# Kernel optimization log

Measured on AMD Instinct MI355X. Metric: run time of the kernel, lower is better.

The kernel has to match this reference:

```python
import jax, jax.numpy as jnp
import numpy as np

N_NODES = 100000

def _sage(x, src, tgt, Wl, bl, Wr):
    # PyG SAGEConv (mean aggr): out = lin_l(mean_{j in N(i)} x_j) + lin_r(x_i)
    msg = x[src]                                             # [E, F] gather
    s = jax.ops.segment_sum(msg, tgt, num_segments=N_NODES)  # [N, F]
    cnt = jax.ops.segment_sum(jnp.ones((src.shape[0], 1), x.dtype), tgt, num_segments=N_NODES)
    agg = s / jnp.maximum(cnt, 1.0)
    return agg @ Wl + bl + x @ Wr


def setup_inputs() -> dict:
    key = jax.random.key(0)
    ks = jax.random.split(key, 16)
    node_dim, edge_dim, hidden = 128, 16, 64
    E = 1000000
    x = jax.random.normal(ks[0], (N_NODES, node_dim), jnp.float32)
    edge_index = jax.random.randint(ks[1], (2, E), 0, N_NODES, jnp.int64)
    edge_attr = jax.random.normal(ks[2], (E, edge_dim), jnp.float32)
    def lin(k, fi, fo, scale=None):
        s = scale if scale is not None else 1.0 / np.sqrt(fi)
        return jax.random.uniform(k, (fi, fo), jnp.float32, -s, s)
    return {
        "x": x, "edge_index": edge_index, "edge_attr": edge_attr,
        # edge MLP: Linear(16,64) -> ReLU -> Linear(64,64)
        "We1": lin(ks[3], edge_dim, hidden), "be1": jnp.zeros((hidden,), jnp.float32),
        "We2": lin(ks[4], hidden, hidden),   "be2": jnp.zeros((hidden,), jnp.float32),
        # SAGEConv 0: lin_l (with bias, on aggregated) + lin_r (no bias, on root)
        "Wl0": lin(ks[5], node_dim, hidden), "bl0": jnp.zeros((hidden,), jnp.float32),
        "Wr0": lin(ks[6], node_dim, hidden),
        # SAGEConv 1
        "Wl1": lin(ks[7], hidden, hidden), "bl1": jnp.zeros((hidden,), jnp.float32),
        "Wr1": lin(ks[8], hidden, hidden),
        # output MLP: Linear(64,64) -> ReLU -> (Dropout eval=id) -> Linear(64,1)
        "Wo1": lin(ks[9], hidden, hidden), "bo1": jnp.zeros((hidden,), jnp.float32),
        "Wo2": lin(ks[10], hidden, 1),     "bo2": jnp.zeros((1,), jnp.float32),
    }


def reference(x, edge_index, edge_attr, We1, be1, We2, be2,
              Wl0, bl0, Wr0, Wl1, bl1, Wr1, Wo1, bo1, Wo2, bo2):
    src, tgt = edge_index[0], edge_index[1]
    # edge MLP (dropout in eval mode = identity)
    ea = jax.nn.relu(edge_attr @ We1 + be1) @ We2 + be2       # [E, H]
    # two SAGE layers with ReLU
    h = jax.nn.relu(_sage(x, src, tgt, Wl0, bl0, Wr0))        # [N, H]
    h = jax.nn.relu(_sage(h, src, tgt, Wl1, bl1, Wr1))        # [N, H]
    # per-edge features: gather both endpoints + edge embedding
    ef = h[src] + h[tgt] + ea                                 # [E, H]
    out = jax.nn.relu(ef @ Wo1 + bo1) @ Wo2 + bo2             # [E, 1]
    return jax.nn.sigmoid(out[:, 0])                          # [E]
```

## Files before the change

kernel.cpp:

```cpp
#include <hip/hip_runtime.h>
#include <math.h>

typedef __attribute__((ext_vector_type(8))) short short8;
typedef __attribute__((ext_vector_type(4))) float f32x4;

#define CAPB 4096

static __device__ __forceinline__ unsigned short f2bf(float f) {
  union { float f; unsigned int u; } x; x.f = f;
  unsigned int r = x.u + 0x7fffu + ((x.u >> 16) & 1u);
  return (unsigned short)(r >> 16);
}
static __device__ __forceinline__ float bf2f(unsigned int u) {
  union { unsigned int u; float f; } x; x.u = u << 16; return x.f;
}

__global__ __launch_bounds__(256) void k_pre(
    const unsigned int* __restrict__ w, int nSample,
    unsigned int* __restrict__ flag, int* __restrict__ gcursor,
    const float* __restrict__ Wl0, const float* __restrict__ Wr0,
    const float* __restrict__ Wl1, const float* __restrict__ Wr1,
    unsigned short* __restrict__ WnT1, unsigned short* __restrict__ WnT0) {
  const int tid = threadIdx.x;
  const int b = blockIdx.x;
  if (b == 0) {
    gcursor[tid] = 0; gcursor[tid + 256] = 0;
    __shared__ unsigned int red[256];
    unsigned int v = 0;
    for (int i = tid; i < nSample; i += 256) v |= w[2 * i + 1];
    red[tid] = v;
    __syncthreads();
    for (int s = 128; s > 0; s >>= 1) {
      if (tid < s) red[tid] |= red[tid + s];
      __syncthreads();
    }
    if (tid == 0) flag[0] = red[0];
  } else if (b <= 32) {
    int idx = (b - 1) * 256 + tid;
    int n = idx >> 6, k = idx & 63;
    float v = (n < 64) ? Wl1[(size_t)k * 64 + n] : Wr1[(size_t)k * 64 + (n - 64)];
    WnT1[idx] = f2bf(v);
  } else {
    int idx = (b - 33) * 256 + tid;
    int n = idx >> 7, k = idx & 127;
    float v = (n < 64) ? Wl0[(size_t)k * 64 + n] : Wr0[(size_t)k * 64 + (n - 64)];
    WnT0[idx] = f2bf(v);
  }
}

template <int K, bool BF16IN, int NTILES>
__device__ __forceinline__ void ngemm_body(
    const void* __restrict__ Xv, const unsigned short* __restrict__ WnT,
    unsigned short* __restrict__ Y0, unsigned short* __restrict__ Y1,
    int N, int blk, unsigned short* __restrict__ sX) {
  constexpr int STR = K + 8;
  constexpr int NC = K / 32;
  const int tid = threadIdx.x;
  const int wv = tid >> 6, lane = tid & 63;
  const int m = lane & 15, q = lane >> 4;
  const int row0 = blk * 64;

  short8 bB[NTILES][NC];
#pragma unroll
  for (int ct = 0; ct < NTILES; ++ct)
#pragma unroll
    for (int c = 0; c < NC; ++c) {
      int n = (NTILES == 2) ? (wv * 32 + ct * 16 + m) : (wv * 16 + m);
      bB[ct][c] = *(const short8*)(WnT + (size_t)n * K + c * 32 + q * 8);
    }

#pragma unroll
  for (int i = 0; i < K / 16; ++i) {
    int f = tid + 256 * i;
    int r = f / (K / 4);
    int c4 = f % (K / 4);
    int rr = row0 + r; if (rr >= N) rr = N - 1;
    uint2 pk;
    if constexpr (BF16IN) {
      pk = *(const uint2*)((const unsigned short*)Xv + (size_t)rr * K + c4 * 4);
    } else {
      float4 v = *(const float4*)((const float*)Xv + (size_t)rr * K + c4 * 4);
      pk.x = (unsigned int)f2bf(v.x) | ((unsigned int)f2bf(v.y) << 16);
      pk.y = (unsigned int)f2bf(v.z) | ((unsigned int)f2bf(v.w) << 16);
    }
    *(uint2*)(sX + r * STR + c4 * 4) = pk;
  }
  __syncthreads();

  f32x4 acc[4][NTILES];
#pragma unroll
  for (int rt = 0; rt < 4; ++rt)
#pragma unroll
    for (int ct = 0; ct < NTILES; ++ct)
#pragma unroll
      for (int r = 0; r < 4; ++r) acc[rt][ct][r] = 0.f;

#pragma unroll
  for (int c = 0; c < NC; ++c) {
    short8 a[4];
#pragma unroll
    for (int rt = 0; rt < 4; ++rt)
      a[rt] = *(const short8*)(sX + (rt * 16 + m) * STR + c * 32 + q * 8);
#pragma unroll
    for (int rt = 0; rt < 4; ++rt)
#pragma unroll
      for (int ct = 0; ct < NTILES; ++ct)
        acc[rt][ct] = __builtin_amdgcn_mfma_f32_16x16x32_bf16(a[rt], bB[ct][c], acc[rt][ct], 0, 0, 0);
  }

#pragma unroll
  for (int rt = 0; rt < 4; ++rt)
#pragma unroll
    for (int ct = 0; ct < NTILES; ++ct) {
      unsigned short* Yw;
      int n;
      if constexpr (NTILES == 2) {
        Yw = (wv < 2) ? Y0 : Y1;
        n = (wv & 1) * 32 + ct * 16 + m;
      } else {
        Yw = Y0;
        n = wv * 16 + m;
      }
#pragma unroll
      for (int reg = 0; reg < 4; ++reg) {
        int row = row0 + rt * 16 + q * 4 + reg;
        if (row < N) Yw[(size_t)row * 64 + n] = f2bf(acc[rt][ct][reg]);
      }
    }
}

template <int K, bool BF16IN, int NTILES>
__global__ __launch_bounds__(256) void k_ngemm(
    const void* __restrict__ Xv, const unsigned short* __restrict__ WnT,
    unsigned short* __restrict__ Y0, unsigned short* __restrict__ Y1, int N) {
  __shared__ __align__(16) unsigned short sX[64 * (K + 8)];
  ngemm_body<K, BF16IN, NTILES>(Xv, WnT, Y0, Y1, N, blockIdx.x, sX);
}

__global__ __launch_bounds__(256) void k_mega1(
    const unsigned int* __restrict__ w, const unsigned int* __restrict__ flag,
    int E, int nDec, int gB,
    int* __restrict__ src, int* __restrict__ tgt,
    int* __restrict__ gcursor, unsigned int* __restrict__ tmp,
    const float* __restrict__ x, const unsigned short* __restrict__ WnT0,
    unsigned short* __restrict__ Yl, unsigned short* __restrict__ Yr, int N,
    const float* __restrict__ We2, const float* __restrict__ Wo1,
    const float* __restrict__ be2, const float* __restrict__ bo1,
    const float* __restrict__ We1,
    unsigned short* __restrict__ W25T, unsigned short* __restrict__ We1T,
    unsigned short* __restrict__ Wo1T, float* __restrict__ cvec,
    const float4* __restrict__ ef, uint2* __restrict__ eb) {
  __shared__ __align__(16) char smem[64 * 136 * 2];
  const int tid = threadIdx.x;
  const int wi = blockIdx.x;

  if (wi < gB) {
    ngemm_body<128, false, 2>(x, WnT0, Yl, Yr, N, wi, (unsigned short*)smem);
    return;
  }
  if (wi < gB + nDec) {
    const int di = wi - gB;
    int* hist = (int*)smem;
    hist[tid] = 0; hist[tid + 256] = 0;
    __syncthreads();
    const int e0 = di * 2048;
    const int e1 = (e0 + 2048 < E) ? (e0 + 2048) : E;
    const unsigned int fl = flag[0];
    for (int e = e0 + tid; e < e1; e += 256) {
      int s, t;
      if (fl) { s = (int)w[e]; t = (int)w[E + e]; }
      else    { s = (int)w[2 * e]; t = (int)w[2 * (E + e)]; }
      src[e] = s; tgt[e] = t;
      atomicAdd(hist + (t >> 8), 1);
    }
    __syncthreads();
    {
      int c0 = hist[tid], c1 = hist[tid + 256];
      int s0 = (c0 > 0) ? atomicAdd(gcursor + tid, c0) : 0;
      int s1 = (c1 > 0) ? atomicAdd(gcursor + tid + 256, c1) : 0;
      __syncthreads();
      hist[tid] = s0; hist[tid + 256] = s1;
    }
    __syncthreads();
    for (int e = e0 + tid; e < e1; e += 256) {
      int s, t;
      if (fl) { s = (int)w[e]; t = (int)w[E + e]; }
      else    { s = (int)w[2 * e]; t = (int)w[2 * (E + e)]; }
      int b = t >> 8;
      int pos = atomicAdd(hist + b, 1);
      if (pos < CAPB)
        tmp[(size_t)b * CAPB + pos] = ((unsigned int)s << 8) | (unsigned int)(t & 255);
    }
    return;
  }
  if (wi == gB + nDec) {
    float* sB = (float*)smem;
    for (int i = tid; i < 1024; i += 256)
      *(float4*)&sB[i * 4] = *(const float4*)(Wo1 + i * 4);
    __syncthreads();
    for (int idx = tid; idx < 4096; idx += 256) {
      int k = idx >> 6, n = idx & 63;
      float s = 0.f;
#pragma unroll 8
      for (int mm = 0; mm < 64; ++mm) s = fmaf(We2[k * 64 + mm], sB[mm * 64 + n], s);
      W25T[n * 64 + k] = f2bf(s);
      Wo1T[n * 64 + k] = f2bf(sB[k * 64 + n]);
    }
    for (int idx = tid; idx < 2048; idx += 256) {
      int n = idx >> 5, k = idx & 31;
      We1T[n * 32 + k] = (k < 16) ? f2bf(We1[k * 64 + n]) : (unsigned short)0;
    }
    if (tid < 64) {
      float s = bo1[tid];
#pragma unroll 8
      for (int mm = 0; mm < 64; ++mm) s = fmaf(be2[mm], sB[mm * 64 + tid], s);
      cvec[tid] = s;
    }
    return;
  }
  const int ci = wi - (gB + nDec + 1);
  const int nItems = E * 4;
#pragma unroll
  for (int j = 0; j < 4; ++j) {
    int i = ci * 1024 + j * 256 + tid;
    if (i < nItems) {
      float4 v = ef[i];
      uint2 pk;
      pk.x = (unsigned int)f2bf(v.x) | ((unsigned int)f2bf(v.y) << 16);
      pk.y = (unsigned int)f2bf(v.z) | ((unsigned int)f2bf(v.w) << 16);
      eb[i] = pk;
    }
  }
}

__global__ __launch_bounds__(256) void k_bsort(
    const unsigned int* __restrict__ tmp, const int* __restrict__ gcursor,
    int* __restrict__ csrc, uint2* __restrict__ rowptr2, int N) {
  __shared__ int cnt[256];
  __shared__ int curs[256];
  __shared__ int wsum[4];
  const int b = blockIdx.x, tid = threadIdx.x;
  int c = gcursor[b]; if (c > CAPB) c = CAPB;
  cnt[tid] = 0;
  __syncthreads();
  const unsigned int* reg = tmp + (size_t)b * CAPB;
  for (int i = tid; i < c; i += 256) atomicAdd(&cnt[reg[i] & 255u], 1);
  __syncthreads();
  const int lane = tid & 63, wv = tid >> 6;
  int v = cnt[tid];
  int incl = v;
#pragma unroll
  for (int off = 1; off < 64; off <<= 1) {
    int t = __shfl_up(incl, off, 64);
    if (lane >= off) incl += t;
  }
  if (lane == 63) wsum[wv] = incl;
  __syncthreads();
  int add = 0;
  for (int ww = 0; ww < wv; ++ww) add += wsum[ww];
  int excl = add + incl - v;
  curs[tid] = excl;
  int node = b * 256 + tid;
  if (node < N)
    rowptr2[node] = make_uint2((unsigned int)(b * CAPB + excl),
                               (unsigned int)(b * CAPB + excl + v));
  __syncthreads();
  for (int i = tid; i < c; i += 256) {
    unsigned int wd = reg[i];
    int p = atomicAdd(&curs[wd & 255u], 1);
    csrc[(size_t)b * CAPB + p] = (int)(wd >> 8);
  }
}

__global__ __launch_bounds__(256) void k_agg(
    const unsigned short* __restrict__ Y, const uint2* __restrict__ rowptr2,
    const int* __restrict__ csrc, const float* __restrict__ bias,
    const unsigned short* __restrict__ Yr, unsigned short* __restrict__ H,
    int N) {
  int node = (blockIdx.x * 256 + threadIdx.x) >> 6;
  if (node >= N) return;
  const int lane = threadIdx.x & 63;
  const int c4 = lane & 15, rr = lane >> 4;
  uint2 be = rowptr2[node];
  int beg = (int)be.x, end = (int)be.y;
  float a0 = 0.f, a1 = 0.f, a2 = 0.f, a3 = 0.f;
  float b0 = 0.f, b1 = 0.f, b2 = 0.f, b3 = 0.f;
  for (int e = beg; e < end; e += 8) {
    int e0 = e + rr, e1 = e + 4 + rr;
    if (e0 < end) {
      int s = csrc[e0];
      uint2 v = *(const uint2*)(Y + (size_t)s * 64 + c4 * 4);
      a0 += bf2f(v.x & 0xffffu); a1 += bf2f(v.x >> 16);
      a2 += bf2f(v.y & 0xffffu); a3 += bf2f(v.y >> 16);
    }
    if (e1 < end) {
      int s = csrc[e1];
      uint2 v = *(const uint2*)(Y + (size_t)s * 64 + c4 * 4);
      b0 += bf2f(v.x & 0xffffu); b1 += bf2f(v.x >> 16);
      b2 += bf2f(v.y & 0xffffu); b3 += bf2f(v.y >> 16);
    }
  }
  a0 += b0; a1 += b1; a2 += b2; a3 += b3;
#pragma unroll
  for (int msk = 16; msk <= 32; msk <<= 1) {
    a0 += __shfl_xor(a0, msk, 64);
    a1 += __shfl_xor(a1, msk, 64);
    a2 += __shfl_xor(a2, msk, 64);
    a3 += __shfl_xor(a3, msk, 64);
  }
  if (rr == 0) {
    float cdeg = (float)(end - beg);
    if (cdeg < 1.f) cdeg = 1.f;
    float inv = 1.f / cdeg;
    float4 bv = *(const float4*)(bias + c4 * 4);
    uint2 yv = *(const uint2*)(Yr + (size_t)node * 64 + c4 * 4);
    float o0 = fmaxf(a0 * inv + bv.x + bf2f(yv.x & 0xffffu), 0.f);
    float o1 = fmaxf(a1 * inv + bv.y + bf2f(yv.x >> 16), 0.f);
    float o2 = fmaxf(a2 * inv + bv.z + bf2f(yv.y & 0xffffu), 0.f);
    float o3 = fmaxf(a3 * inv + bv.w + bf2f(yv.y >> 16), 0.f);
    uint2 pk;
    pk.x = (unsigned int)f2bf(o0) | ((unsigned int)f2bf(o1) << 16);
    pk.y = (unsigned int)f2bf(o2) | ((unsigned int)f2bf(o3) << 16);
    *(uint2*)(H + (size_t)node * 64 + c4 * 4) = pk;
  }
}

#define T1_STRIDE 72
#define G_STRIDE 68
__global__ __launch_bounds__(256) void k_edge3(
    const unsigned short* __restrict__ EAb, const int* __restrict__ src,
    const int* __restrict__ tgt, const unsigned short* __restrict__ Gb,
    const unsigned short* __restrict__ We1T,
    const unsigned short* __restrict__ W25T,
    const float* __restrict__ cvec, const float* __restrict__ be1,
    const float* __restrict__ Wo2, const float* __restrict__ bo2,
    float* __restrict__ out, int E, int nT, int nWaves) {
  __shared__ __align__(16) char sBuf[4][4352];
  const int tid = threadIdx.x;
  const int wid = tid >> 6, lane = tid & 63;
  const int m = lane & 15, q = lane >> 4;
  unsigned short* sT1 = (unsigned short*)sBuf[wid];
  float* sG = (float*)sBuf[wid];

  short8 bWe1[4], bW25[4][2];
  float cv[4], wo2v[4], be1v[4];
#pragma unroll
  for (int nt = 0; nt < 4; ++nt) {
    int n = nt * 16 + m;
    bWe1[nt] = *(const short8*)(We1T + n * 32 + q * 8);
    bW25[nt][0] = *(const short8*)(W25T + n * 64 + q * 8);
    bW25[nt][1] = *(const short8*)(W25T + n * 64 + 32 + q * 8);
    cv[nt] = cvec[n];
    wo2v[nt] = Wo2[n];
    be1v[nt] = be1[n];
  }
  const float b_out = bo2[0];
  const short8 zfrag = {};

  int t = blockIdx.x * 4 + wid;
  if (t >= nT) return;

  uint2 sv[4], tv[4];
  {
    int il = t * 16 + m; if (il >= E) il = E - 1;
    int my = (lane < 16) ? src[il] : ((lane < 32) ? tgt[il] : 0);
#pragma unroll
    for (int r = 0; r < 4; ++r) {
      int a = __shfl(my, q * 4 + r, 64);
      int b = __shfl(my, 16 + q * 4 + r, 64);
      sv[r] = *(const uint2*)(Gb + (size_t)a * 64 + m * 4);
      tv[r] = *(const uint2*)(Gb + (size_t)b * 64 + m * 4);
    }
  }

  while (true) {
    const int base = t * 16;
    const int tn = t + nWaves;
    const bool last = (tn >= nT);
    const int tc = last ? t : tn;

    int il_n = tc * 16 + m; if (il_n >= E) il_n = E - 1;
    int idx_n = (lane < 16) ? src[il_n] : ((lane < 32) ? tgt[il_n] : 0);
    uint2 sv_n[4], tv_n[4];
#pragma unroll
    for (int r = 0; r < 4; ++r) {
      int a = __shfl(idx_n, q * 4 + r, 64);
      int b = __shfl(idx_n, 16 + q * 4 + r, 64);
      sv_n[r] = *(const uint2*)(Gb + (size_t)a * 64 + m * 4);
      tv_n[r] = *(const uint2*)(Gb + (size_t)b * 64 + m * 4);
    }

    int er = base + m; if (er >= E) er = E - 1;
    short8 aEA = zfrag;
    if (q < 2) aEA = *(const short8*)(EAb + (size_t)er * 16 + (q & 1) * 8);

    f32x4 t1[4];
#pragma unroll
    for (int nt = 0; nt < 4; ++nt) {
      f32x4 cinit; cinit[0] = be1v[nt]; cinit[1] = be1v[nt];
      cinit[2] = be1v[nt]; cinit[3] = be1v[nt];
      t1[nt] = __builtin_amdgcn_mfma_f32_16x16x32_bf16(aEA, bWe1[nt], cinit, 0, 0, 0);
    }
#pragma unroll
    for (int nt = 0; nt < 4; ++nt)
#pragma unroll
      for (int r = 0; r < 4; ++r)
        sT1[(q * 4 + r) * T1_STRIDE + nt * 16 + m] = f2bf(fmaxf(t1[nt][r], 0.f));
    short8 aT0 = *(short8*)(sT1 + m * T1_STRIDE + q * 8);
    short8 aT1 = *(short8*)(sT1 + m * T1_STRIDE + 32 + q * 8);

#pragma unroll
    for (int r = 0; r < 4; ++r) {
      f32x4 g;
      g[0] = bf2f(sv[r].x & 0xffffu) + bf2f(tv[r].x & 0xffffu);
      g[1] = bf2f(sv[r].x >> 16)     + bf2f(tv[r].x >> 16);
      g[2] = bf2f(sv[r].y & 0xffffu) + bf2f(tv[r].y & 0xffffu);
      g[3] = bf2f(sv[r].y >> 16)     + bf2f(tv[r].y >> 16);
      *(f32x4*)(sG + (q * 4 + r) * G_STRIDE + m * 4) = g;
    }

    f32x4 acc[4];
#pragma unroll
    for (int nt = 0; nt < 4; ++nt)
#pragma unroll
      for (int r = 0; r < 4; ++r)
        acc[nt][r] = cv[nt] + sG[(q * 4 + r) * G_STRIDE + nt * 16 + m];
#pragma unroll
    for (int nt = 0; nt < 4; ++nt) {
      acc[nt] = __builtin_amdgcn_mfma_f32_16x16x32_bf16(aT0, bW25[nt][0], acc[nt], 0, 0, 0);
      acc[nt] = __builtin_amdgcn_mfma_f32_16x16x32_bf16(aT1, bW25[nt][1], acc[nt], 0, 0, 0);
    }

    float p[4];
#pragma unroll
    for (int r = 0; r < 4; ++r) {
      p[r] = fmaxf(acc[0][r], 0.f) * wo2v[0] + fmaxf(acc[1][r], 0.f) * wo2v[1] +
             fmaxf(acc[2][r], 0.f) * wo2v[2] + fmaxf(acc[3][r], 0.f) * wo2v[3];
    }
#pragma unroll
    for (int msk = 1; msk <= 8; msk <<= 1) {
#pragma unroll
      for (int r = 0; r < 4; ++r) p[r] += __shfl_xor(p[r], msk, 64);
    }
    if (m == 0) {
#pragma unroll
      for (int r = 0; r < 4; ++r) {
        int row = base + q * 4 + r;
        if (row < E) out[row] = 1.f / (1.f + __expf(-(p[r] + b_out)));
      }
    }

    if (last) break;
    t = tn;
#pragma unroll
    for (int r = 0; r < 4; ++r) { sv[r] = sv_n[r]; tv[r] = tv_n[r]; }
  }
}

extern "C" void kernel_launch(void* const* d_in, const int* in_sizes, int n_in,
                              void* d_out, int out_size, void* d_ws, size_t ws_size,
                              hipStream_t stream) {
  const float* x     = (const float*)d_in[0];
  const unsigned int* eidx = (const unsigned int*)d_in[1];
  const float* eattr = (const float*)d_in[2];
  const float* We1 = (const float*)d_in[3];
  const float* be1 = (const float*)d_in[4];
  const float* We2 = (const float*)d_in[5];
  const float* be2 = (const float*)d_in[6];
  const float* Wl0 = (const float*)d_in[7];
  const float* bl0 = (const float*)d_in[8];
  const float* Wr0 = (const float*)d_in[9];
  const float* Wl1 = (const float*)d_in[10];
  const float* bl1 = (const float*)d_in[11];
  const float* Wr1 = (const float*)d_in[12];
  const float* Wo1 = (const float*)d_in[13];
  const float* bo1 = (const float*)d_in[14];
  const float* Wo2 = (const float*)d_in[15];
  const float* bo2 = (const float*)d_in[16];

  const int N = in_sizes[0] / 128;
  const int E = in_sizes[2] / 16;
  const int NBUCK = (N + 255) >> 8;
  float* out = (float*)d_out;

  char* ws = (char*)d_ws;
  size_t off = 0;
  auto alloc = [&](size_t bytes) {
    char* p = ws + off;
    off += (bytes + 255) & ~(size_t)255;
    return p;
  };
  unsigned int* flag = (unsigned int*)alloc(256);
  int* src    = (int*)alloc((size_t)E * 4);
  int* tgt    = (int*)alloc((size_t)E * 4);
  int* gcursor = (int*)alloc(512 * 4);
  unsigned int* tmp = (unsigned int*)alloc((size_t)NBUCK * CAPB * 4);
  int* csrc   = (int*)alloc((size_t)NBUCK * CAPB * 4);
  uint2* rowptr2 = (uint2*)alloc((size_t)N * 8);
  unsigned short* EAb = (unsigned short*)alloc((size_t)E * 16 * 2);
  unsigned short* Hb = (unsigned short*)alloc((size_t)N * 64 * 2);
  unsigned short* Yl = (unsigned short*)alloc((size_t)N * 64 * 2);
  unsigned short* Yr = (unsigned short*)alloc((size_t)N * 64 * 2);
  unsigned short* Gb = (unsigned short*)alloc((size_t)N * 64 * 2);
  unsigned short* W25T = (unsigned short*)alloc(64 * 64 * 2);
  unsigned short* We1T = (unsigned short*)alloc(64 * 32 * 2);
  unsigned short* Wo1T = (unsigned short*)alloc(64 * 64 * 2);
  unsigned short* WnT1 = (unsigned short*)alloc(128 * 64 * 2);
  unsigned short* WnT0 = (unsigned short*)alloc(128 * 128 * 2);
  float* cvec = (float*)alloc(64 * 4);
  (void)ws_size; (void)n_in; (void)out_size;

  const int nDec = (E + 2047) / 2048;
  const int gB = (N + 63) / 64;
  const int nConv = (E * 4 + 1023) / 1024;

  k_pre<<<97, 256, 0, stream>>>(eidx, 8192, flag, gcursor,
                                Wl0, Wr0, Wl1, Wr1, WnT1, WnT0);

  k_mega1<<<gB + nDec + 1 + nConv, 256, 0, stream>>>(
      eidx, flag, E, nDec, gB,
      src, tgt, gcursor, tmp,
      x, WnT0, Yl, Yr, N,
      We2, Wo1, be2, bo1, We1,
      W25T, We1T, Wo1T, cvec,
      (const float4*)eattr, (uint2*)EAb);

  k_bsort<<<NBUCK, 256, 0, stream>>>(tmp, gcursor, csrc, rowptr2, N);

  const int aggB = (N + 3) / 4;
  k_agg<<<aggB, 256, 0, stream>>>(Yl, rowptr2, csrc, bl0, Yr, Hb, N);

  k_ngemm<64, true, 2><<<gB, 256, 0, stream>>>(Hb, WnT1, Yl, Yr, N);
  k_agg<<<aggB, 256, 0, stream>>>(Yl, rowptr2, csrc, bl1, Yr, Hb, N);

  k_ngemm<64, true, 1><<<gB, 256, 0, stream>>>(Hb, Wo1T, Gb, nullptr, N);

  const int nT = (E + 15) / 16;
  const int blocks = 3072;
  k_edge3<<<blocks, 256, 0, stream>>>(EAb, src, tgt, Gb, We1T, W25T, cvec,
                                      be1, Wo2, bo2, out, E, nT, blocks * 4);
}
```

Baseline: 429.6 us.

## Fuse SAGE mean aggregation with following node GEMM and drop edge gather prefetch

Mean-neighbour aggregation is merged with the next dense bf16 MFMA projection in one kernel. Aggregated rows go into shared memory instead of an H buffer in global memory, which removes two launches and an N×64 write and read per layer, with new ping-pong Yl2/Yr2 buffers. Each wave now aggregates 16 nodes one after another, so there is less parallelism across nodes and 64-row blocks may be load-imbalanced. The edge kernel stops prefetching next-tile Gb rows into registers and loads them in the same iteration, lowering register pressure but exposing gather latency; it also splits its shared buffer into separate T1 and G arrays.

```diff
diff --git a/kernel.cpp b/kernel.cpp
--- a/kernel.cpp
+++ b/kernel.cpp
@@ -129,14 +129,6 @@
     }
 }
 
-template <int K, bool BF16IN, int NTILES>
-__global__ __launch_bounds__(256) void k_ngemm(
-    const void* __restrict__ Xv, const unsigned short* __restrict__ WnT,
-    unsigned short* __restrict__ Y0, unsigned short* __restrict__ Y1, int N) {
-  __shared__ __align__(16) unsigned short sX[64 * (K + 8)];
-  ngemm_body<K, BF16IN, NTILES>(Xv, WnT, Y0, Y1, N, blockIdx.x, sX);
-}
-
 __global__ __launch_bounds__(256) void k_mega1(
     const unsigned int* __restrict__ w, const unsigned int* __restrict__ flag,
     int E, int nDec, int gB,
@@ -272,57 +264,122 @@
   }
 }
 
-__global__ __launch_bounds__(256) void k_agg(
+template <int NTILES>
+__global__ __launch_bounds__(256) void k_fagg(
     const unsigned short* __restrict__ Y, const uint2* __restrict__ rowptr2,
     const int* __restrict__ csrc, const float* __restrict__ bias,
-    const unsigned short* __restrict__ Yr, unsigned short* __restrict__ H,
-    int N) {
-  int node = (blockIdx.x * 256 + threadIdx.x) >> 6;
-  if (node >= N) return;
-  const int lane = threadIdx.x & 63;
-  const int c4 = lane & 15, rr = lane >> 4;
-  uint2 be = rowptr2[node];
-  int beg = (int)be.x, end = (int)be.y;
-  float a0 = 0.f, a1 = 0.f, a2 = 0.f, a3 = 0.f;
-  float b0 = 0.f, b1 = 0.f, b2 = 0.f, b3 = 0.f;
-  for (int e = beg; e < end; e += 8) {
-    int e0 = e + rr, e1 = e + 4 + rr;
-    if (e0 < end) {
-      int s = csrc[e0];
-      uint2 v = *(const uint2*)(Y + (size_t)s * 64 + c4 * 4);
-      a0 += bf2f(v.x & 0xffffu); a1 += bf2f(v.x >> 16);
-      a2 += bf2f(v.y & 0xffffu); a3 += bf2f(v.y >> 16);
-    }
-    if (e1 < end) {
-      int s = csrc[e1];
-      uint2 v = *(const uint2*)(Y + (size_t)s * 64 + c4 * 4);
-      b0 += bf2f(v.x & 0xffffu); b1 += bf2f(v.x >> 16);
-      b2 += bf2f(v.y & 0xffffu); b3 += bf2f(v.y >> 16);
-    }
-  }
-  a0 += b0; a1 += b1; a2 += b2; a3 += b3;
-#pragma unroll
-  for (int msk = 16; msk <= 32; msk <<= 1) {
-    a0 += __shfl_xor(a0, msk, 64);
-    a1 += __shfl_xor(a1, msk, 64);
-    a2 += __shfl_xor(a2, msk, 64);
-    a3 += __shfl_xor(a3, msk, 64);
-  }
-  if (rr == 0) {
-    float cdeg = (float)(end - beg);
-    if (cdeg < 1.f) cdeg = 1.f;
-    float inv = 1.f / cdeg;
-    float4 bv = *(const float4*)(bias + c4 * 4);
-    uint2 yv = *(const uint2*)(Yr + (size_t)node * 64 + c4 * 4);
-    float o0 = fmaxf(a0 * inv + bv.x + bf2f(yv.x & 0xffffu), 0.f);
-    float o1 = fmaxf(a1 * inv + bv.y + bf2f(yv.x >> 16), 0.f);
-    float o2 = fmaxf(a2 * inv + bv.z + bf2f(yv.y & 0xffffu), 0.f);
-    float o3 = fmaxf(a3 * inv + bv.w + bf2f(yv.y >> 16), 0.f);
-    uint2 pk;
-    pk.x = (unsigned int)f2bf(o0) | ((unsigned int)f2bf(o1) << 16);
-    pk.y = (unsigned int)f2bf(o2) | ((unsigned int)f2bf(o3) << 16);
-    *(uint2*)(H + (size_t)node * 64 + c4 * 4) = pk;
-  }
+    const unsigned short* __restrict__ Yr, const unsigned short* __restrict__ WnT,
+    unsigned short* __restrict__ Y0, unsigned short* __restrict__ Y1, int N) {
+  constexpr int K = 64;
+  constexpr int STR = K + 8;
+  constexpr int NC = K / 32;
+  __shared__ __align__(16) unsigned short sX[64 * STR];
+  const int tid = threadIdx.x;
+  const int wv = tid >> 6, lane = tid & 63;
+  const int m = lane & 15, q = lane >> 4;
+  const int row0 = blockIdx.x * 64;
+
+  short8 bB[NTILES][NC];
+#pragma unroll
+  for (int ct = 0; ct < NTILES; ++ct)
+#pragma unroll
+    for (int c = 0; c < NC; ++c) {
+      int n = (NTILES == 2) ? (wv * 32 + ct * 16 + m) : (wv * 16 + m);
+      bB[ct][c] = *(const short8*)(WnT + (size_t)n * K + c * 32 + q * 8);
+    }
+
+  {
+    int nb = row0 + wv * 16 + m; if (nb >= N) nb = N - 1;
+    uint2 myrp = rowptr2[nb];
+    float4 bv = *(const float4*)(bias + m * 4);
+    for (int i = 0; i < 16; ++i) {
+      int r = wv * 16 + i;
+      int node = row0 + r; if (node >= N) node = N - 1;
+      int beg = __shfl((int)myrp.x, i, 16);
+      int end = __shfl((int)myrp.y, i, 16);
+      float a0 = 0.f, a1 = 0.f, a2 = 0.f, a3 = 0.f;
+      float b0 = 0.f, b1 = 0.f, b2 = 0.f, b3 = 0.f;
+      for (int e = beg; e < end; e += 8) {
+        int e0 = e + q, e1 = e + 4 + q;
+        if (e0 < end) {
+          int s = csrc[e0];
+          uint2 v = *(const uint2*)(Y + (size_t)s * 64 + m * 4);
+          a0 += bf2f(v.x & 0xffffu); a1 += bf2f(v.x >> 16);
+          a2 += bf2f(v.y & 0xffffu); a3 += bf2f(v.y >> 16);
+        }
+        if (e1 < end) {
+          int s = csrc[e1];
+          uint2 v = *(const uint2*)(Y + (size_t)s * 64 + m * 4);
+          b0 += bf2f(v.x & 0xffffu); b1 += bf2f(v.x >> 16);
+          b2 += bf2f(v.y & 0xffffu); b3 += bf2f(v.y >> 16);
+        }
+      }
+      a0 += b0; a1 += b1; a2 += b2; a3 += b3;
+#pragma unroll
+      for (int msk = 16; msk <= 32; msk <<= 1) {
+        a0 += __shfl_xor(a0, msk, 64);
+        a1 += __shfl_xor(a1, msk, 64);
+        a2 += __shfl_xor(a2, msk, 64);
+        a3 += __shfl_xor(a3, msk, 64);
+      }
+      if (q == 0) {
+        float cdeg = (float)(end - beg);
+        if (cdeg < 1.f) cdeg = 1.f;
+        float inv = 1.f / cdeg;
+        uint2 yv = *(const uint2*)(Yr + (size_t)node * 64 + m * 4);
+        float o0 = fmaxf(a0 * inv + bv.x + bf2f(yv.x & 0xffffu), 0.f);
+        float o1 = fmaxf(a1 * inv + bv.y + bf2f(yv.x >> 16), 0.f);
+        float o2 = fmaxf(a2 * inv + bv.z + bf2f(yv.y & 0xffffu), 0.f);
+        float o3 = fmaxf(a3 * inv + bv.w + bf2f(yv.y >> 16), 0.f);
+        uint2 pk;
+        pk.x = (unsigned int)f2bf(o0) | ((unsigned int)f2bf(o1) << 16);
+        pk.y = (unsigned int)f2bf(o2) | ((unsigned int)f2bf(o3) << 16);
+        *(uint2*)(sX + r * STR + m * 4) = pk;
+      }
+    }
+  }
+  __syncthreads();
+
+  f32x4 acc[4][NTILES];
+#pragma unroll
+  for (int rt = 0; rt < 4; ++rt)
+#pragma unroll
+    for (int ct = 0; ct < NTILES; ++ct)
+#pragma unroll
+      for (int r = 0; r < 4; ++r) acc[rt][ct][r] = 0.f;
+
+#pragma unroll
+  for (int c = 0; c < NC; ++c) {
+    short8 a[4];
+#pragma unroll
+    for (int rt = 0; rt < 4; ++rt)
+      a[rt] = *(const short8*)(sX + (rt * 16 + m) * STR + c * 32 + q * 8);
+#pragma unroll
+    for (int rt = 0; rt < 4; ++rt)
+#pragma unroll
+      for (int ct = 0; ct < NTILES; ++ct)
+        acc[rt][ct] = __builtin_amdgcn_mfma_f32_16x16x32_bf16(a[rt], bB[ct][c], acc[rt][ct], 0, 0, 0);
+  }
+
+#pragma unroll
+  for (int rt = 0; rt < 4; ++rt)
+#pragma unroll
+    for (int ct = 0; ct < NTILES; ++ct) {
+      unsigned short* Yw;
+      int n;
+      if constexpr (NTILES == 2) {
+        Yw = (wv < 2) ? Y0 : Y1;
+        n = (wv & 1) * 32 + ct * 16 + m;
+      } else {
+        Yw = Y0;
+        n = wv * 16 + m;
+      }
+#pragma unroll
+      for (int reg = 0; reg < 4; ++reg) {
+        int row = row0 + rt * 16 + q * 4 + reg;
+        if (row < N) Yw[(size_t)row * 64 + n] = f2bf(acc[rt][ct][reg]);
+      }
+    }
 }
 
 #define T1_STRIDE 72
@@ -335,12 +392,13 @@
     const float* __restrict__ cvec, const float* __restrict__ be1,
     const float* __restrict__ Wo2, const float* __restrict__ bo2,
     float* __restrict__ out, int E, int nT, int nWaves) {
-  __shared__ __align__(16) char sBuf[4][4352];
+  __shared__ unsigned short sT1a[4][16 * T1_STRIDE];
+  __shared__ float sGa[4][16 * G_STRIDE];
   const int tid = threadIdx.x;
   const int wid = tid >> 6, lane = tid & 63;
   const int m = lane & 15, q = lane >> 4;
-  unsigned short* sT1 = (unsigned short*)sBuf[wid];
-  float* sG = (float*)sBuf[wid];
+  unsigned short* sT1 = sT1a[wid];
+  float* sG = sGa[wid];
 
   short8 bWe1[4], bW25[4][2];
   float cv[4], wo2v[4], be1v[4];
@@ -359,19 +417,8 @@
 
   int t = blockIdx.x * 4 + wid;
   if (t >= nT) return;
-
-  uint2 sv[4], tv[4];
-  {
-    int il = t * 16 + m; if (il >= E) il = E - 1;
-    int my = (lane < 16) ? src[il] : ((lane < 32) ? tgt[il] : 0);
-#pragma unroll
-    for (int r = 0; r < 4; ++r) {
-      int a = __shfl(my, q * 4 + r, 64);
-      int b = __shfl(my, 16 + q * 4 + r, 64);
-      sv[r] = *(const uint2*)(Gb + (size_t)a * 64 + m * 4);
-      tv[r] = *(const uint2*)(Gb + (size_t)b * 64 + m * 4);
-    }
-  }
+  int il = t * 16 + m; if (il >= E) il = E - 1;
+  int my_idx = (lane < 16) ? src[il] : ((lane < 32) ? tgt[il] : 0);
 
   while (true) {
     const int base = t * 16;
@@ -381,13 +428,18 @@
 
     int il_n = tc * 16 + m; if (il_n >= E) il_n = E - 1;
     int idx_n = (lane < 16) ? src[il_n] : ((lane < 32) ? tgt[il_n] : 0);
-    uint2 sv_n[4], tv_n[4];
+
+    int rs[4], rt[4];
 #pragma unroll
     for (int r = 0; r < 4; ++r) {
-      int a = __shfl(idx_n, q * 4 + r, 64);
-      int b = __shfl(idx_n, 16 + q * 4 + r, 64);
-      sv_n[r] = *(const uint2*)(Gb + (size_t)a * 64 + m * 4);
-      tv_n[r] = *(const uint2*)(Gb + (size_t)b * 64 + m * 4);
+      rs[r] = __shfl(my_idx, q * 4 + r, 64);
+      rt[r] = __shfl(my_idx, 16 + q * 4 + r, 64);
+    }
+    uint2 sv[4], tv[4];
+#pragma unroll
+    for (int r = 0; r < 4; ++r) {
+      sv[r] = *(const uint2*)(Gb + (size_t)rs[r] * 64 + m * 4);
+      tv[r] = *(const uint2*)(Gb + (size_t)rt[r] * 64 + m * 4);
     }
 
     int er = base + m; if (er >= E) er = E - 1;
@@ -451,9 +503,7 @@
     }
 
     if (last) break;
-    t = tn;
-#pragma unroll
-    for (int r = 0; r < 4; ++r) { sv[r] = sv_n[r]; tv[r] = tv_n[r]; }
+    t = tn; my_idx = idx_n;
   }
 }
 
@@ -498,9 +548,10 @@
   int* csrc   = (int*)alloc((size_t)NBUCK * CAPB * 4);
   uint2* rowptr2 = (uint2*)alloc((size_t)N * 8);
   unsigned short* EAb = (unsigned short*)alloc((size_t)E * 16 * 2);
-  unsigned short* Hb = (unsigned short*)alloc((size_t)N * 64 * 2);
   unsigned short* Yl = (unsigned short*)alloc((size_t)N * 64 * 2);
   unsigned short* Yr = (unsigned short*)alloc((size_t)N * 64 * 2);
+  unsigned short* Yl2 = (unsigned short*)alloc((size_t)N * 64 * 2);
+  unsigned short* Yr2 = (unsigned short*)alloc((size_t)N * 64 * 2);
   unsigned short* Gb = (unsigned short*)alloc((size_t)N * 64 * 2);
   unsigned short* W25T = (unsigned short*)alloc(64 * 64 * 2);
   unsigned short* We1T = (unsigned short*)alloc(64 * 32 * 2);
@@ -527,13 +578,10 @@
 
   k_bsort<<<NBUCK, 256, 0, stream>>>(tmp, gcursor, csrc, rowptr2, N);
 
-  const int aggB = (N + 3) / 4;
-  k_agg<<<aggB, 256, 0, stream>>>(Yl, rowptr2, csrc, bl0, Yr, Hb, N);
-
-  k_ngemm<64, true, 2><<<gB, 256, 0, stream>>>(Hb, WnT1, Yl, Yr, N);
-  k_agg<<<aggB, 256, 0, stream>>>(Yl, rowptr2, csrc, bl1, Yr, Hb, N);
-
-  k_ngemm<64, true, 1><<<gB, 256, 0, stream>>>(Hb, Wo1T, Gb, nullptr, N);
+  k_fagg<2><<<gB, 256, 0, stream>>>(Yl, rowptr2, csrc, bl0, Yr, WnT1,
+                                    Yl2, Yr2, N);
+  k_fagg<1><<<gB, 256, 0, stream>>>(Yl2, rowptr2, csrc, bl1, Yr2, Wo1T,
+                                    Gb, nullptr, N);
 
   const int nT = (E + 15) / 16;
   const int blocks = 3072;
```

Result: no change. 431.7 us (+0.5%).

## Fuse bucket sort into aggregation using LDS float atomics per bucket half

Applied to the files above, without the earlier changes.

Drops the CSR build kernel (k_bsort) and the per-node gather aggregation. A new k_bagg kernel scans each 256-node bucket's edge list directly and accumulates neighbour features into shared memory with float atomics, split across two blocks per bucket (128 nodes each). It then writes mean+bias+root output. This removes a kernel launch and the csrc/rowptr writes and reads, at the cost of each half-block reading the whole bucket list and heavy LDS atomic contention. Floating-point summation order also becomes nondeterministic. Separately, the edge kernel drops its register-level prefetch of the next tile's gathered rows and uses split LDS buffers.

```diff
diff --git a/kernel.cpp b/kernel.cpp
--- a/kernel.cpp
+++ b/kernel.cpp
@@ -233,95 +233,72 @@
   }
 }
 
-__global__ __launch_bounds__(256) void k_bsort(
+__global__ __launch_bounds__(256) void k_bagg(
     const unsigned int* __restrict__ tmp, const int* __restrict__ gcursor,
-    int* __restrict__ csrc, uint2* __restrict__ rowptr2, int N) {
-  __shared__ int cnt[256];
-  __shared__ int curs[256];
-  __shared__ int wsum[4];
-  const int b = blockIdx.x, tid = threadIdx.x;
-  int c = gcursor[b]; if (c > CAPB) c = CAPB;
-  cnt[tid] = 0;
-  __syncthreads();
-  const unsigned int* reg = tmp + (size_t)b * CAPB;
-  for (int i = tid; i < c; i += 256) atomicAdd(&cnt[reg[i] & 255u], 1);
-  __syncthreads();
-  const int lane = tid & 63, wv = tid >> 6;
-  int v = cnt[tid];
-  int incl = v;
-#pragma unroll
-  for (int off = 1; off < 64; off <<= 1) {
-    int t = __shfl_up(incl, off, 64);
-    if (lane >= off) incl += t;
-  }
-  if (lane == 63) wsum[wv] = incl;
-  __syncthreads();
-  int add = 0;
-  for (int ww = 0; ww < wv; ++ww) add += wsum[ww];
-  int excl = add + incl - v;
-  curs[tid] = excl;
-  int node = b * 256 + tid;
-  if (node < N)
-    rowptr2[node] = make_uint2((unsigned int)(b * CAPB + excl),
-                               (unsigned int)(b * CAPB + excl + v));
-  __syncthreads();
-  for (int i = tid; i < c; i += 256) {
-    unsigned int wd = reg[i];
-    int p = atomicAdd(&curs[wd & 255u], 1);
-    csrc[(size_t)b * CAPB + p] = (int)(wd >> 8);
-  }
-}
-
-__global__ __launch_bounds__(256) void k_agg(
-    const unsigned short* __restrict__ Y, const uint2* __restrict__ rowptr2,
-    const int* __restrict__ csrc, const float* __restrict__ bias,
+    const unsigned short* __restrict__ Y, const float* __restrict__ bias,
     const unsigned short* __restrict__ Yr, unsigned short* __restrict__ H,
     int N) {
-  int node = (blockIdx.x * 256 + threadIdx.x) >> 6;
-  if (node >= N) return;
-  const int lane = threadIdx.x & 63;
-  const int c4 = lane & 15, rr = lane >> 4;
-  uint2 be = rowptr2[node];
-  int beg = (int)be.x, end = (int)be.y;
-  float a0 = 0.f, a1 = 0.f, a2 = 0.f, a3 = 0.f;
-  float b0 = 0.f, b1 = 0.f, b2 = 0.f, b3 = 0.f;
-  for (int e = beg; e < end; e += 8) {
-    int e0 = e + rr, e1 = e + 4 + rr;
-    if (e0 < end) {
-      int s = csrc[e0];
-      uint2 v = *(const uint2*)(Y + (size_t)s * 64 + c4 * 4);
-      a0 += bf2f(v.x & 0xffffu); a1 += bf2f(v.x >> 16);
-      a2 += bf2f(v.y & 0xffffu); a3 += bf2f(v.y >> 16);
-    }
-    if (e1 < end) {
-      int s = csrc[e1];
-      uint2 v = *(const uint2*)(Y + (size_t)s * 64 + c4 * 4);
-      b0 += bf2f(v.x & 0xffffu); b1 += bf2f(v.x >> 16);
-      b2 += bf2f(v.y & 0xffffu); b3 += bf2f(v.y >> 16);
-    }
-  }
-  a0 += b0; a1 += b1; a2 += b2; a3 += b3;
-#pragma unroll
-  for (int msk = 16; msk <= 32; msk <<= 1) {
-    a0 += __shfl_xor(a0, msk, 64);
-    a1 += __shfl_xor(a1, msk, 64);
-    a2 += __shfl_xor(a2, msk, 64);
-    a3 += __shfl_xor(a3, msk, 64);
-  }
-  if (rr == 0) {
-    float cdeg = (float)(end - beg);
-    if (cdeg < 1.f) cdeg = 1.f;
-    float inv = 1.f / cdeg;
-    float4 bv = *(const float4*)(bias + c4 * 4);
-    uint2 yv = *(const uint2*)(Yr + (size_t)node * 64 + c4 * 4);
-    float o0 = fmaxf(a0 * inv + bv.x + bf2f(yv.x & 0xffffu), 0.f);
-    float o1 = fmaxf(a1 * inv + bv.y + bf2f(yv.x >> 16), 0.f);
-    float o2 = fmaxf(a2 * inv + bv.z + bf2f(yv.y & 0xffffu), 0.f);
-    float o3 = fmaxf(a3 * inv + bv.w + bf2f(yv.y >> 16), 0.f);
-    uint2 pk;
-    pk.x = (unsigned int)f2bf(o0) | ((unsigned int)f2bf(o1) << 16);
-    pk.y = (unsigned int)f2bf(o2) | ((unsigned int)f2bf(o3) << 16);
-    *(uint2*)(H + (size_t)node * 64 + c4 * 4) = pk;
+  __shared__ float acc[128 * 65];
+  __shared__ int cnt[128];
+  const int tid = threadIdx.x;
+  const int b = blockIdx.x >> 1, h = blockIdx.x & 1;
+  const int g = tid >> 4, m = tid & 15;
+  for (int i = tid; i < 128 * 65; i += 256) acc[i] = 0.f;
+  if (tid < 128) cnt[tid] = 0;
+  __syncthreads();
+
+  int c = gcursor[b]; if (c > CAPB) c = CAPB;
+  const unsigned int* reg = tmp + (size_t)b * CAPB;
+  for (int e = g; e < c; e += 32) {
+    unsigned int w0 = reg[e];
+    int e1i = e + 16;
+    bool v1 = (e1i < c);
+    unsigned int w1 = v1 ? reg[e1i] : 0u;
+    int tl0 = (int)(w0 & 255u), tl1 = (int)(w1 & 255u);
+    bool p0 = ((tl0 >> 7) == h);
+    bool p1 = v1 && ((tl1 >> 7) == h);
+    uint2 y0, y1;
+    if (p0) y0 = *(const uint2*)(Y + (size_t)(w0 >> 8) * 64 + m * 4);
+    if (p1) y1 = *(const uint2*)(Y + (size_t)(w1 >> 8) * 64 + m * 4);
+    if (p0) {
+      float* a = acc + (tl0 & 127) * 65 + m * 4;
+      atomicAdd(a + 0, bf2f(y0.x & 0xffffu));
+      atomicAdd(a + 1, bf2f(y0.x >> 16));
+      atomicAdd(a + 2, bf2f(y0.y & 0xffffu));
+      atomicAdd(a + 3, bf2f(y0.y >> 16));
+      if (m == 0) atomicAdd(&cnt[tl0 & 127], 1);
+    }
+    if (p1) {
+      float* a = acc + (tl1 & 127) * 65 + m * 4;
+      atomicAdd(a + 0, bf2f(y1.x & 0xffffu));
+      atomicAdd(a + 1, bf2f(y1.x >> 16));
+      atomicAdd(a + 2, bf2f(y1.y & 0xffffu));
+      atomicAdd(a + 3, bf2f(y1.y >> 16));
+      if (m == 0) atomicAdd(&cnt[tl1 & 127], 1);
+    }
+  }
+  __syncthreads();
+
+#pragma unroll
+  for (int it = 0; it < 8; ++it) {
+    int idx = it * 256 + tid;
+    int nl = idx >> 4, cq = idx & 15;
+    int node = b * 256 + h * 128 + nl;
+    if (node < N) {
+      float cd = (float)cnt[nl]; if (cd < 1.f) cd = 1.f;
+      float inv = 1.f / cd;
+      const float* a = acc + nl * 65 + cq * 4;
+      float4 bv = *(const float4*)(bias + cq * 4);
+      uint2 yv = *(const uint2*)(Yr + (size_t)node * 64 + cq * 4);
+      float o0 = fmaxf(a[0] * inv + bv.x + bf2f(yv.x & 0xffffu), 0.f);
+      float o1 = fmaxf(a[1] * inv + bv.y + bf2f(yv.x >> 16), 0.f);
+      float o2 = fmaxf(a[2] * inv + bv.z + bf2f(yv.y & 0xffffu), 0.f);
+      float o3 = fmaxf(a[3] * inv + bv.w + bf2f(yv.y >> 16), 0.f);
+      uint2 pk;
+      pk.x = (unsigned int)f2bf(o0) | ((unsigned int)f2bf(o1) << 16);
+      pk.y = (unsigned int)f2bf(o2) | ((unsigned int)f2bf(o3) << 16);
+      *(uint2*)(H + (size_t)node * 64 + cq * 4) = pk;
+    }
   }
 }
 
@@ -335,12 +312,13 @@
     const float* __restrict__ cvec, const float* __restrict__ be1,
     const float* __restrict__ Wo2, const float* __restrict__ bo2,
     float* __restrict__ out, int E, int nT, int nWaves) {
-  __shared__ __align__(16) char sBuf[4][4352];
+  __shared__ unsigned short sT1a[4][16 * T1_STRIDE];
+  __shared__ float sGa[4][16 * G_STRIDE];
   const int tid = threadIdx.x;
   const int wid = tid >> 6, lane = tid & 63;
   const int m = lane & 15, q = lane >> 4;
-  unsigned short* sT1 = (unsigned short*)sBuf[wid];
-  float* sG = (float*)sBuf[wid];
+  unsigned short* sT1 = sT1a[wid];
+  float* sG = sGa[wid];
 
   short8 bWe1[4], bW25[4][2];
   float cv[4], wo2v[4], be1v[4];
@@ -359,19 +337,8 @@
 
   int t = blockIdx.x * 4 + wid;
   if (t >= nT) return;
-
-  uint2 sv[4], tv[4];
-  {
-    int il = t * 16 + m; if (il >= E) il = E - 1;
-    int my = (lane < 16) ? src[il] : ((lane < 32) ? tgt[il] : 0);
-#pragma unroll
-    for (int r = 0; r < 4; ++r) {
-      int a = __shfl(my, q * 4 + r, 64);
-      int b = __shfl(my, 16 + q * 4 + r, 64);
-      sv[r] = *(const uint2*)(Gb + (size_t)a * 64 + m * 4);
-      tv[r] = *(const uint2*)(Gb + (size_t)b * 64 + m * 4);
-    }
-  }
+  int il = t * 16 + m; if (il >= E) il = E - 1;
+  int my_idx = (lane < 16) ? src[il] : ((lane < 32) ? tgt[il] : 0);
 
   while (true) {
     const int base = t * 16;
@@ -381,13 +348,18 @@
 
     int il_n = tc * 16 + m; if (il_n >= E) il_n = E - 1;
     int idx_n = (lane < 16) ? src[il_n] : ((lane < 32) ? tgt[il_n] : 0);
-    uint2 sv_n[4], tv_n[4];
+
+    int rs[4], rt[4];
 #pragma unroll
     for (int r = 0; r < 4; ++r) {
-      int a = __shfl(idx_n, q * 4 + r, 64);
-      int b = __shfl(idx_n, 16 + q * 4 + r, 64);
-      sv_n[r] = *(const uint2*)(Gb + (size_t)a * 64 + m * 4);
-      tv_n[r] = *(const uint2*)(Gb + (size_t)b * 64 + m * 4);
+      rs[r] = __shfl(my_idx, q * 4 + r, 64);
+      rt[r] = __shfl(my_idx, 16 + q * 4 + r, 64);
+    }
+    uint2 sv[4], tv[4];
+#pragma unroll
+    for (int r = 0; r < 4; ++r) {
+      sv[r] = *(const uint2*)(Gb + (size_t)rs[r] * 64 + m * 4);
+      tv[r] = *(const uint2*)(Gb + (size_t)rt[r] * 64 + m * 4);
     }
 
     int er = base + m; if (er >= E) er = E - 1;
@@ -451,9 +423,7 @@
     }
 
     if (last) break;
-    t = tn;
-#pragma unroll
-    for (int r = 0; r < 4; ++r) { sv[r] = sv_n[r]; tv[r] = tv_n[r]; }
+    t = tn; my_idx = idx_n;
   }
 }
 
@@ -495,12 +465,12 @@
   int* tgt    = (int*)alloc((size_t)E * 4);
   int* gcursor = (int*)alloc(512 * 4);
   unsigned int* tmp = (unsigned int*)alloc((size_t)NBUCK * CAPB * 4);
-  int* csrc   = (int*)alloc((size_t)NBUCK * CAPB * 4);
-  uint2* rowptr2 = (uint2*)alloc((size_t)N * 8);
   unsigned short* EAb = (unsigned short*)alloc((size_t)E * 16 * 2);
   unsigned short* Hb = (unsigned short*)alloc((size_t)N * 64 * 2);
   unsigned short* Yl = (unsigned short*)alloc((size_t)N * 64 * 2);
   unsigned short* Yr = (unsigned short*)alloc((size_t)N * 64 * 2);
+  unsigned short* Yl2 = (unsigned short*)alloc((size_t)N * 64 * 2);
+  unsigned short* Yr2 = (unsigned short*)alloc((size_t)N * 64 * 2);
   unsigned short* Gb = (unsigned short*)alloc((size_t)N * 64 * 2);
   unsigned short* W25T = (unsigned short*)alloc(64 * 64 * 2);
   unsigned short* We1T = (unsigned short*)alloc(64 * 32 * 2);
@@ -525,14 +495,10 @@
       W25T, We1T, Wo1T, cvec,
       (const float4*)eattr, (uint2*)EAb);
 
-  k_bsort<<<NBUCK, 256, 0, stream>>>(tmp, gcursor, csrc, rowptr2, N);
-
-  const int aggB = (N + 3) / 4;
-  k_agg<<<aggB, 256, 0, stream>>>(Yl, rowptr2, csrc, bl0, Yr, Hb, N);
-
-  k_ngemm<64, true, 2><<<gB, 256, 0, stream>>>(Hb, WnT1, Yl, Yr, N);
-  k_agg<<<aggB, 256, 0, stream>>>(Yl, rowptr2, csrc, bl1, Yr, Hb, N);
-
+  k_bagg<<<NBUCK * 2, 256, 0, stream>>>(tmp, gcursor, Yl, bl0, Yr, Hb, N);
+  k_ngemm<64, true, 2><<<gB, 256, 0, stream>>>(Hb, WnT1, Yl2, Yr2, N);
+
+  k_bagg<<<NBUCK * 2, 256, 0, stream>>>(tmp, gcursor, Yl2, bl1, Yr2, Hb, N);
   k_ngemm<64, true, 1><<<gB, 256, 0, stream>>>(Hb, Wo1T, Gb, nullptr, N);
 
   const int nT = (E + 15) / 16;
```

After: 1.168 ms. 2.72x slower.
